# Kernel tuning notes

Hardware: AMD Instinct MI355X
Metric: run time of the kernel (lower is better)

The kernel has to match this reference:

```python
import jax, jax.numpy as jnp
import numpy as np

K, P, Q, D = 16, 1024, 1024, 64  # heads, value-in dim, out dim, head dim; P'=P, Q'=Q, D'=D
B, N = 2, 2048                   # batch, seq (self-attention: M=N)
TEMPERATURE = jnp.sqrt(jnp.float32(D))

def _xavier(key, shape):
    fan_in, fan_out = shape[-2], shape[-1]
    lim = jnp.sqrt(6.0 / (fan_in + fan_out))
    return jax.random.uniform(key, shape, jnp.float32, -lim, lim)

def setup_inputs() -> dict:
    key = jax.random.key(0)
    k0, k1, k2, k3, k4 = jax.random.split(key, 5)
    return {
        'y_prime': jax.random.normal(k0, (B, N, Q), jnp.float32),
        'mask': jnp.zeros((N, N), jnp.float32),  # log-domain additive mask [M,N]
        'Lam_x': _xavier(k1, (K, P, D)),  # Lambda^(x): [K,P',D']
        'Lam_y': _xavier(k2, (K, Q, D)),  # Lambda^(y): [K,Q',D']
        'Th_x': _xavier(k3, (K, P, D)),   # Theta^(x):  [K,P,D]
        'Th_y': _xavier(k4, (K, Q, D)),   # Theta^(y):  [K,Q,D]
    }

def reference(y_prime, mask, Lam_x, Lam_y, Th_x, Th_y):
    # self-attention: x' = x = y'
    x_p = y_prime
    x = x_p
    # key projection: [B,M,K,D']
    r = jnp.einsum('bmp,kpd->bmkd', x_p, Lam_x)
    # bilinear scores: [K,B,M,N]
    r = jnp.einsum('bmkd,kqd,bnq->kbmn', r, Lam_y, y_prime)
    r = r + mask[None, None, :, :]
    # softmax over M (axis=-2), scaled by sqrt(D')
    A = jax.nn.softmax(r / TEMPERATURE, axis=-2)
    # value aggregation: [B,N,K,D]
    r = jnp.einsum('kbmn,bmp,kpd->bnkd', A, x, Th_x)
    # output projection: [B,N,Q]
    return jnp.einsum('bnkd,kqd->bnq', r, Th_y)
```

## Files before the change

kernel.cpp:

```cpp
#include <hip/hip_runtime.h>
#include <hip/hip_bf16.h>

#define KH 16
#define PD 1024
#define QD 1024
#define DD 64
#define BB 2
#define NN 2048
#define BN 4096
#define ST 72
#define SOFT_C 12.0f
#define LOG2E 1.4426950408889634f
#define SOFT_C2 17.312340490667560f

typedef unsigned short u16;
typedef __attribute__((ext_vector_type(8))) short bf16x8;
typedef __attribute__((ext_vector_type(4))) short bf16x4;
typedef __attribute__((ext_vector_type(4))) float f32x4;

__device__ __forceinline__ float bf2f(u16 u) {
    return __uint_as_float(((unsigned)u) << 16);
}
__device__ __forceinline__ u16 f2bf(float f) {
    unsigned x = __float_as_uint(f);
    x += 0x7FFFu + ((x >> 16) & 1u);
    return (u16)(x >> 16);
}
__device__ __forceinline__ f32x4 mfma_k32(bf16x8 a, bf16x8 b, f32x4 c) {
    return __builtin_amdgcn_mfma_f32_16x16x32_bf16(a, b, c, 0, 0, 0);
}
__device__ __forceinline__ bf16x8 ldfrag(const u16* base, int r0, int kc, int lane) {
    return *reinterpret_cast<const bf16x8*>(base + (r0 + (lane & 15)) * ST + kc +
                                            ((lane >> 4) << 3));
}
__device__ __forceinline__ bf16x8 ldfragL(const u16* base, int r0, int kc, int lane) {
    return *reinterpret_cast<const bf16x8*>(base + ((r0 + (lane & 15)) << 6) + kc +
                                            ((lane >> 4) << 3));
}
__device__ __forceinline__ bf16x4 pack4(float a, float b, float c, float d) {
    union { bf16x4 v; __hip_bfloat162 h[2]; } u;
    u.h[0] = __float22bfloat162_rn(make_float2(a, b));
    u.h[1] = __float22bfloat162_rn(make_float2(c, d));
    return u.v;
}
__device__ __forceinline__ void gl_lds16(const u16* g, u16* l) {
    __builtin_amdgcn_global_load_lds(
        (const __attribute__((address_space(1))) void*)g,
        (__attribute__((address_space(3))) void*)l, 16, 0, 0);
}
template <int ROWS>
__device__ __forceinline__ void stage_dma(const u16* __restrict__ src, int ld,
                                          u16* dst, int lane, int w) {
#pragma unroll
    for (int c = 0; c < ROWS / 32; ++c) {
        int rbase = (w * (ROWS / 32) + c) * 8;
        const u16* g = src + (size_t)(rbase + (lane >> 3)) * ld + ((lane & 7) << 3);
        gl_lds16(g, dst + (rbase << 6));
    }
}

__global__ void detect_kernel(const u16* __restrict__ y, int* flag, int* mnz) {
    __shared__ int cnt;
    if (threadIdx.x == 0) cnt = 0;
    __syncthreads();
    int local = 0;
    for (int i = threadIdx.x; i < 8192; i += 256) {
        u16 u = y[i];
        int e = (u >> 7) & 0xFF;
        if (u == 0 || (e >= 96 && e < 160)) local++;
    }
    atomicAdd(&cnt, local);
    __syncthreads();
    if (threadIdx.x == 0) {
        *flag = (cnt > 7372) ? 1 : 0;
        *mnz = 0;
    }
}

__global__ __launch_bounds__(256) void prep_kernel(
    const void* __restrict__ ysrc, const void* __restrict__ msrc,
    const void* __restrict__ s0, const void* __restrict__ s1,
    const void* __restrict__ s2, const void* __restrict__ s3,
    u16* __restrict__ ycan, u16* __restrict__ LamXt, u16* __restrict__ LamYt,
    u16* __restrict__ ThXt, u16* __restrict__ ThYr, u16* __restrict__ maskc,
    const int* __restrict__ flag, int* __restrict__ mnz) {
    int z = blockIdx.z, bx = blockIdx.x, tid = threadIdx.x;
    int isbf = *flag;
    if (z == 0) {
        size_t n4 = (size_t)NN * NN / 8;
        if (!isbf) n4 *= 2;
        const uint4* p = (const uint4*)msrc;
        unsigned acc = 0;
        for (size_t i = (size_t)bx * 256 + tid; i < n4; i += 256 * 256) {
            uint4 v = p[i];
            acc |= v.x | v.y | v.z | v.w;
        }
        if (acc) atomicOr(mnz, 1);
    } else if (z == 1) {
        int n = BN * PD;
        for (int i = (bx * 256 + tid) * 4; i < n; i += 256 * 256 * 4) {
            if (isbf) {
                *reinterpret_cast<uint2*>(ycan + i) =
                    *reinterpret_cast<const uint2*>((const u16*)ysrc + i);
            } else {
                float4 f = *reinterpret_cast<const float4*>((const float*)ysrc + i);
                u16 t[4] = {f2bf(f.x), f2bf(f.y), f2bf(f.z), f2bf(f.w)};
                *reinterpret_cast<uint2*>(ycan + i) = *reinterpret_cast<uint2*>(t);
            }
        }
    } else if (z <= 4) {
        const void* src = (z == 2) ? s0 : (z == 3) ? s1 : s2;
        u16* dst = (z == 2) ? LamXt : (z == 3) ? LamYt : ThXt;
        float scale = (z == 3) ? 0.125f : 1.0f;
        int k = bx >> 4, p0 = (bx & 15) * 64;
        __shared__ float T[64][65];
        const u16* s16 = (const u16*)src + ((size_t)k * PD + p0) * DD;
        const float* s32 = (const float*)src + ((size_t)k * PD + p0) * DD;
#pragma unroll
        for (int it = 0; it < 2; ++it) {
            int chunk = it * 256 + tid;
            int row = chunk >> 3, c8 = (chunk & 7) << 3;
            float f[8];
            if (isbf) {
                uint4 v = *reinterpret_cast<const uint4*>(s16 + row * DD + c8);
                u16 t[8];
                *reinterpret_cast<uint4*>(t) = v;
#pragma unroll
                for (int e = 0; e < 8; ++e) f[e] = bf2f(t[e]);
            } else {
                float4 a = *reinterpret_cast<const float4*>(s32 + row * DD + c8);
                float4 b = *reinterpret_cast<const float4*>(s32 + row * DD + c8 + 4);
                f[0] = a.x; f[1] = a.y; f[2] = a.z; f[3] = a.w;
                f[4] = b.x; f[5] = b.y; f[6] = b.z; f[7] = b.w;
            }
#pragma unroll
            for (int e = 0; e < 8; ++e) T[row][c8 + e] = f[e] * scale;
        }
        __syncthreads();
        u16* drow = dst + (size_t)k * DD * PD + p0;
#pragma unroll
        for (int it = 0; it < 2; ++it) {
            int chunk = it * 256 + tid;
            int d = chunk >> 3, c8 = (chunk & 7) << 3;
            u16 t[8];
#pragma unroll
            for (int e = 0; e < 8; ++e) t[e] = f2bf(T[c8 + e][d]);
            *reinterpret_cast<uint4*>(drow + (size_t)d * PD + c8) =
                *reinterpret_cast<uint4*>(t);
        }
    } else if (z == 5) {
        int k = bx >> 4, q0 = (bx & 15) * 64;
#pragma unroll
        for (int it = 0; it < 2; ++it) {
            int chunk = it * 256 + tid;
            int row = chunk >> 3, c8 = (chunk & 7) << 3;
            size_t si = ((size_t)k * QD + q0 + row) * DD + c8;
            u16 t[8];
            if (isbf) {
                *reinterpret_cast<uint4*>(t) =
                    *reinterpret_cast<const uint4*>((const u16*)s3 + si);
            } else {
                float4 a = *reinterpret_cast<const float4*>((const float*)s3 + si);
                float4 b = *reinterpret_cast<const float4*>((const float*)s3 + si + 4);
                t[0] = f2bf(a.x); t[1] = f2bf(a.y); t[2] = f2bf(a.z); t[3] = f2bf(a.w);
                t[4] = f2bf(b.x); t[5] = f2bf(b.y); t[6] = f2bf(b.z); t[7] = f2bf(b.w);
            }
            *reinterpret_cast<uint4*>(ThYr + (size_t)(q0 + row) * (KH * DD) +
                                      k * DD + c8) = *reinterpret_cast<uint4*>(t);
        }
    } else {
        size_t n8 = (size_t)NN * NN / 8;
        for (size_t c = (size_t)bx * 256 + tid; c < n8; c += 256 * 256) {
            size_t i = c * 8;
            float f[8];
            if (isbf) {
                uint4 v = *reinterpret_cast<const uint4*>((const u16*)msrc + i);
                u16 t[8];
                *reinterpret_cast<uint4*>(t) = v;
#pragma unroll
                for (int e = 0; e < 8; ++e) f[e] = bf2f(t[e]);
            } else {
                float4 a = *reinterpret_cast<const float4*>((const float*)msrc + i);
                float4 b = *reinterpret_cast<const float4*>((const float*)msrc + i + 4);
                f[0] = a.x; f[1] = a.y; f[2] = a.z; f[3] = a.w;
                f[4] = b.x; f[5] = b.y; f[6] = b.z; f[7] = b.w;
            }
            u16 t[8];
#pragma unroll
            for (int e = 0; e < 8; ++e) t[e] = f2bf(f[e] * 0.125f);
            *reinterpret_cast<uint4*>(maskc + i) = *reinterpret_cast<uint4*>(t);
        }
    }
}

__global__ __launch_bounds__(256, 3) void proj_gemm(
    const u16* __restrict__ A,
    const u16* __restrict__ Bm,
    u16* __restrict__ Xk, u16* __restrict__ Yk, u16* __restrict__ Vtg) {
    int tid = threadIdx.x, lane = tid & 63, w = tid >> 6;
    int mhalf = w & 1, nhalf = w >> 1;
    int m0 = blockIdx.x * 128, n0 = blockIdx.y * 128;
    __shared__ u16 As[128 * 64];
    __shared__ u16 Bs[128 * 64];
    f32x4 acc[4][4] = {};

    for (int kk = 0; kk < PD; kk += 64) {
        __syncthreads();
        stage_dma<128>(A + (size_t)m0 * PD + kk, PD, As, lane, w);
        stage_dma<128>(Bm + (size_t)n0 * PD + kk, PD, Bs, lane, w);
        __syncthreads();
#pragma unroll
        for (int kc = 0; kc < 64; kc += 32) {
            bf16x8 af[4], bf[4];
#pragma unroll
            for (int i = 0; i < 4; ++i) af[i] = ldfragL(As, mhalf * 64 + i * 16, kc, lane);
#pragma unroll
            for (int j = 0; j < 4; ++j) bf[j] = ldfragL(Bs, nhalf * 64 + j * 16, kc, lane);
#pragma unroll
            for (int i = 0; i < 4; ++i)
#pragma unroll
                for (int j = 0; j < 4; ++j) acc[i][j] = mfma_k32(af[i], bf[j], acc[i][j]);
        }
    }
    int s = n0 >> 10;
    int quad = lane >> 4, col = lane & 15;
    u16* stg = nhalf ? Bs : As;
    __syncthreads();
    if (s == 2) {
#pragma unroll
        for (int i = 0; i < 4; ++i)
#pragma unroll
            for (int j = 0; j < 4; ++j)
                *reinterpret_cast<bf16x4*>(stg + ((mhalf * 2 + (i >> 1)) * 4 + j) * 512 +
                                           quad * 128 + col * 8 + (i & 1) * 4) =
                    pack4(acc[i][j][0], acc[i][j][1], acc[i][j][2], acc[i][j][3]);
    } else {
#pragma unroll
        for (int i = 0; i < 4; ++i)
#pragma unroll
            for (int j = 0; j < 4; ++j)
#pragma unroll
                for (int reg = 0; reg < 4; ++reg)
                    stg[(mhalf * 64 + i * 16 + quad * 4 + reg) * 64 + j * 16 + col] =
                        f2bf(acc[i][j][reg]);
    }
    __syncthreads();
#pragma unroll
    for (int h = 0; h < 2; ++h) {
        int kh = ((n0 + h * 64) >> 6) & 15;
        const u16* src = h ? Bs : As;
        if (s == 2) {
            u16* vb = Vtg + (size_t)kh * DD * BN + (size_t)m0 * 64;
#pragma unroll
            for (int it = 0; it < 4; ++it) {
                int chunk = it * 256 + tid;
                *reinterpret_cast<uint4*>(vb + chunk * 8) =
                    *reinterpret_cast<const uint4*>(src + chunk * 8);
            }
        } else {
            u16* ob = (s == 0 ? Xk : Yk) + (size_t)kh * BN * DD + (size_t)m0 * DD;
#pragma unroll
            for (int it = 0; it < 4; ++it) {
                int chunk = it * 256 + tid;
                *reinterpret_cast<uint4*>(ob + chunk * 8) =
                    *reinterpret_cast<const uint4*>(src + chunk * 8);
            }
        }
    }
}

__global__ __launch_bounds__(512, 4) void attn_kernel(
    const u16* __restrict__ Xk,
    const u16* __restrict__ Yk,
    const u16* __restrict__ Vtg,
    const u16* __restrict__ maskc,
    const int* __restrict__ mnz,
    u16* __restrict__ O) {
    int tid = threadIdx.x, lane = tid & 63, w = tid >> 6;
    int quad = lane >> 4, col = lane & 15;
    int H = blockIdx.x;
    int L = (H & 7) * 64 + (H >> 3);
    int q0 = (L & 15) * 128, k = (L >> 4) & 15, b = L >> 8;
    const u16* Qp = Yk + ((size_t)k * BN + b * NN + q0) * DD;
    const u16* Kp = Xk + ((size_t)k * BN + b * NN) * DD;
    const u16* Vh = Vtg + (size_t)k * DD * BN + (size_t)b * NN * 64;
    __shared__ u16 Kb[3][64 * ST];
    __shared__ u16 Ost[128 * ST];
    int mz = *mnz;

    const u16* qrow = Qp + (size_t)(w * 16 + col) * DD + (quad << 3);
    bf16x8 qf0 = *reinterpret_cast<const bf16x8*>(qrow);
    bf16x8 qf1 = *reinterpret_cast<const bf16x8*>(qrow + 32);

    int srow = tid >> 3, scol = (tid & 7) << 3;
    const u16* kgp = Kp + (size_t)srow * DD + scol;
    int soff = srow * ST + scol;

    uint4 kr = *reinterpret_cast<const uint4*>(kgp);
    *reinterpret_cast<uint4*>(Kb[0] + soff) = kr;
    kr = *reinterpret_cast<const uint4*>(kgp + (size_t)64 * DD);
    __syncthreads();

    float lp = 0.0f;
    f32x4 oacc[4] = {};

    for (int t = 0; t < 32; ++t) {
        int cur = t % 3;
        if (t < 31) {
            int nxt = (t + 1) % 3;
            *reinterpret_cast<uint4*>(Kb[nxt] + soff) = kr;
            __syncthreads();
        }
        const u16* Ks = Kb[cur];
        const u16* vt = Vh + t * 4096;
        bf16x8 av[2][4];
#pragma unroll
        for (int half = 0; half < 2; ++half)
#pragma unroll
            for (int dg = 0; dg < 4; ++dg)
                av[half][dg] = *reinterpret_cast<const bf16x8*>(
                    vt + half * 2048 + dg * 512 + lane * 8);
        if (t < 30) kr = *reinterpret_cast<const uint4*>(kgp + (size_t)(t + 2) * 64 * DD);
        int m0 = t * 64;

        bf16x4 pb4[4];
#pragma unroll
        for (int kg = 0; kg < 4; ++kg) {
            bf16x8 a0 = ldfrag(Ks, kg * 16, 0, lane);
            bf16x8 a1 = ldfrag(Ks, kg * 16, 32, lane);
            f32x4 s = {};
            s = mfma_k32(a0, qf0, s);
            s = mfma_k32(a1, qf1, s);
            if (mz) {
#pragma unroll
                for (int reg = 0; reg < 4; ++reg)
                    s[reg] += bf2f(
                        maskc[(size_t)(m0 + kg * 16 + quad * 4 + reg) * NN + q0 +
                              w * 16 + col]);
            }
            float p0 = exp2f(fmaf(s[0], LOG2E, -SOFT_C2));
            float p1 = exp2f(fmaf(s[1], LOG2E, -SOFT_C2));
            float p2 = exp2f(fmaf(s[2], LOG2E, -SOFT_C2));
            float p3 = exp2f(fmaf(s[3], LOG2E, -SOFT_C2));
            lp += (p0 + p1) + (p2 + p3);
            pb4[kg] = pack4(p0, p1, p2, p3);
        }
#pragma unroll
        for (int half = 0; half < 2; ++half) {
            bf16x8 pb8 = __builtin_shufflevector(pb4[half * 2], pb4[half * 2 + 1],
                                                 0, 1, 2, 3, 4, 5, 6, 7);
#pragma unroll
            for (int dg = 0; dg < 4; ++dg)
                oacc[dg] = mfma_k32(av[half][dg], pb8, oacc[dg]);
        }
    }

    float l = lp;
    l += __shfl_xor(l, 16);
    l += __shfl_xor(l, 32);
    float inv = 1.0f / l;
    int q = w * 16 + col;
#pragma unroll
    for (int dg = 0; dg < 4; ++dg)
        *reinterpret_cast<bf16x4*>(Ost + q * ST + dg * 16 + quad * 4) =
            pack4(oacc[dg][0] * inv, oacc[dg][1] * inv, oacc[dg][2] * inv,
                  oacc[dg][3] * inv);
    __syncthreads();
#pragma unroll
    for (int it = 0; it < 2; ++it) {
        int chunk = it * 512 + tid;
        int row = chunk >> 3, c8 = (chunk & 7) << 3;
        *reinterpret_cast<uint4*>(O + (size_t)(b * NN + q0 + row) * (KH * DD) +
                                  k * DD + c8) =
            *reinterpret_cast<const uint4*>(Ost + row * ST + c8);
    }
}

__global__ __launch_bounds__(256, 3) void out_gemm(
    const u16* __restrict__ A,
    const u16* __restrict__ Bm,
    const int* __restrict__ flag,
    void* __restrict__ outv) {
    int tid = threadIdx.x, lane = tid & 63, w = tid >> 6;
    int mhalf = w & 1, nhalf = w >> 1;
    int m0 = blockIdx.x * 128, n0 = blockIdx.y * 128;
    __shared__ u16 S[2][128 * 64];
    u16* As = S[0];
    u16* Bs = S[1];
    f32x4 acc[4][4] = {};

    for (int kk = 0; kk < KH * DD; kk += 64) {
        __syncthreads();
        stage_dma<128>(A + (size_t)m0 * (KH * DD) + kk, KH * DD, As, lane, w);
        stage_dma<128>(Bm + (size_t)n0 * (KH * DD) + kk, KH * DD, Bs, lane, w);
        __syncthreads();
#pragma unroll
        for (int kc = 0; kc < 64; kc += 32) {
            bf16x8 af[4], bf[4];
#pragma unroll
            for (int i = 0; i < 4; ++i) af[i] = ldfragL(As, mhalf * 64 + i * 16, kc, lane);
#pragma unroll
            for (int j = 0; j < 4; ++j) bf[j] = ldfragL(Bs, nhalf * 64 + j * 16, kc, lane);
#pragma unroll
            for (int i = 0; i < 4; ++i)
#pragma unroll
                for (int j = 0; j < 4; ++j) acc[i][j] = mfma_k32(af[i], bf[j], acc[i][j]);
        }
    }
    int isbf = *flag;
    int quad = lane >> 4, col = lane & 15;
    if (isbf) {
#pragma unroll
        for (int i = 0; i < 4; ++i)
#pragma unroll
            for (int j = 0; j < 4; ++j)
#pragma unroll
                for (int reg = 0; reg < 4; ++reg) {
                    size_t row = m0 + mhalf * 64 + i * 16 + quad * 4 + reg;
                    int c = n0 + nhalf * 64 + j * 16 + col;
                    ((u16*)outv)[row * QD + c] = f2bf(acc[i][j][reg]);
                }
    } else {
        float* Sf = (float*)&S[0][0];
#pragma unroll
        for (int h = 0; h < 2; ++h) {
            __syncthreads();
            if (mhalf == h) {
#pragma unroll
                for (int i = 0; i < 4; ++i)
#pragma unroll
                    for (int j = 0; j < 4; ++j)
#pragma unroll
                        for (int reg = 0; reg < 4; ++reg)
                            Sf[(i * 16 + quad * 4 + reg) * 128 + nhalf * 64 +
                               j * 16 + col] = acc[i][j][reg];
            }
            __syncthreads();
            float* orow = (float*)outv + (size_t)(m0 + h * 64) * QD + n0;
#pragma unroll
            for (int it = 0; it < 8; ++it) {
                int chunk = it * 256 + tid;
                int row = chunk >> 5, c4 = (chunk & 31) * 4;
                *reinterpret_cast<float4*>(orow + (size_t)row * QD + c4) =
                    *reinterpret_cast<const float4*>(Sf + row * 128 + c4);
            }
        }
    }
}

extern "C" void kernel_launch(void* const* d_in, const int* in_sizes, int n_in,
                              void* d_out, int out_size, void* d_ws, size_t ws_size,
                              hipStream_t stream) {
    char* wsb = (char*)d_ws;
    int* flag = (int*)wsb;
    int* mnz = (int*)(wsb + 16);
    u16* ycan = (u16*)(wsb + 64);
    const size_t NYP = (size_t)BN * PD;
    const size_t NW = (size_t)KH * PD * DD;
    const size_t OSZ = (size_t)BN * KH * DD;
    u16* Wcat = ycan + NYP;
    u16* ThYr = Wcat + 3 * NW;
    u16* Xk = ThYr + NW;
    u16* Yk = Xk + OSZ;
    u16* Vtg = Yk + OSZ;
    u16* maskc = Vtg + OSZ;
    u16* Ob = ycan;

    detect_kernel<<<1, 256, 0, stream>>>((const u16*)d_in[0], flag, mnz);
    prep_kernel<<<dim3(256, 1, 7), 256, 0, stream>>>(
        d_in[0], d_in[1], d_in[2], d_in[3], d_in[4], d_in[5], ycan, Wcat,
        Wcat + NW, Wcat + 2 * NW, ThYr, maskc, flag, mnz);
    proj_gemm<<<dim3(BN / 128, 3072 / 128), 256, 0, stream>>>(ycan, Wcat, Xk, Yk, Vtg);
    attn_kernel<<<512, 512, 0, stream>>>(Xk, Yk, Vtg, maskc, mnz, Ob);
    out_gemm<<<dim3(BN / 128, QD / 128), 256, 0, stream>>>(Ob, ThYr, flag, d_out);
}
```

Before: 234.2 us.

## Split mask scan, skip zero-mask conversion, shrink attention blocks, raise MFMA priority

Mask-nonzero detection moves into its own kernel that runs before prep, so prep can skip converting the mask when it is all zero. When the input is already bf16, prep skips copying y and proj_gemm reads the source directly. The attention kernel goes from 512-thread blocks covering 128 queries to 256-thread blocks covering 64 queries, with twice as many blocks. Each thread now stages two K rows per tile, and setprio is raised around the PV MFMAs. This trades an extra launch and more K re-reads for less conversion traffic and finer-grained attention scheduling.

Result: no change. 230.9 us (-1.4%).

```diff
diff --git a/kernel.cpp b/kernel.cpp
--- a/kernel.cpp
+++ b/kernel.cpp
@@ -77,41 +77,41 @@
     }
 }
 
+__global__ __launch_bounds__(256) void scan_kernel(const void* __restrict__ msrc,
+                                                   const int* __restrict__ flag,
+                                                   int* __restrict__ mnz) {
+    size_t n4 = (size_t)NN * NN / 8;
+    if (!*flag) n4 *= 2;
+    const uint4* p = (const uint4*)msrc;
+    unsigned acc = 0;
+    for (size_t i = (size_t)blockIdx.x * 256 + threadIdx.x; i < n4; i += 256 * 256) {
+        uint4 v = p[i];
+        acc |= v.x | v.y | v.z | v.w;
+    }
+    if (acc) atomicOr(mnz, 1);
+}
+
 __global__ __launch_bounds__(256) void prep_kernel(
     const void* __restrict__ ysrc, const void* __restrict__ msrc,
     const void* __restrict__ s0, const void* __restrict__ s1,
     const void* __restrict__ s2, const void* __restrict__ s3,
     u16* __restrict__ ycan, u16* __restrict__ LamXt, u16* __restrict__ LamYt,
     u16* __restrict__ ThXt, u16* __restrict__ ThYr, u16* __restrict__ maskc,
-    const int* __restrict__ flag, int* __restrict__ mnz) {
+    const int* __restrict__ flag, const int* __restrict__ mnz) {
     int z = blockIdx.z, bx = blockIdx.x, tid = threadIdx.x;
     int isbf = *flag;
     if (z == 0) {
-        size_t n4 = (size_t)NN * NN / 8;
-        if (!isbf) n4 *= 2;
-        const uint4* p = (const uint4*)msrc;
-        unsigned acc = 0;
-        for (size_t i = (size_t)bx * 256 + tid; i < n4; i += 256 * 256) {
-            uint4 v = p[i];
-            acc |= v.x | v.y | v.z | v.w;
-        }
-        if (acc) atomicOr(mnz, 1);
-    } else if (z == 1) {
+        if (isbf) return;
         int n = BN * PD;
         for (int i = (bx * 256 + tid) * 4; i < n; i += 256 * 256 * 4) {
-            if (isbf) {
-                *reinterpret_cast<uint2*>(ycan + i) =
-                    *reinterpret_cast<const uint2*>((const u16*)ysrc + i);
-            } else {
-                float4 f = *reinterpret_cast<const float4*>((const float*)ysrc + i);
-                u16 t[4] = {f2bf(f.x), f2bf(f.y), f2bf(f.z), f2bf(f.w)};
-                *reinterpret_cast<uint2*>(ycan + i) = *reinterpret_cast<uint2*>(t);
-            }
-        }
-    } else if (z <= 4) {
-        const void* src = (z == 2) ? s0 : (z == 3) ? s1 : s2;
-        u16* dst = (z == 2) ? LamXt : (z == 3) ? LamYt : ThXt;
-        float scale = (z == 3) ? 0.125f : 1.0f;
+            float4 f = *reinterpret_cast<const float4*>((const float*)ysrc + i);
+            u16 t[4] = {f2bf(f.x), f2bf(f.y), f2bf(f.z), f2bf(f.w)};
+            *reinterpret_cast<uint2*>(ycan + i) = *reinterpret_cast<uint2*>(t);
+        }
+    } else if (z <= 3) {
+        const void* src = (z == 1) ? s0 : (z == 2) ? s1 : s2;
+        u16* dst = (z == 1) ? LamXt : (z == 2) ? LamYt : ThXt;
+        float scale = (z == 2) ? 0.125f : 1.0f;
         int k = bx >> 4, p0 = (bx & 15) * 64;
         __shared__ float T[64][65];
         const u16* s16 = (const u16*)src + ((size_t)k * PD + p0) * DD;
@@ -148,7 +148,7 @@
             *reinterpret_cast<uint4*>(drow + (size_t)d * PD + c8) =
                 *reinterpret_cast<uint4*>(t);
         }
-    } else if (z == 5) {
+    } else if (z == 4) {
         int k = bx >> 4, q0 = (bx & 15) * 64;
 #pragma unroll
         for (int it = 0; it < 2; ++it) {
@@ -169,6 +169,7 @@
                                       k * DD + c8) = *reinterpret_cast<uint4*>(t);
         }
     } else {
+        if (*mnz == 0) return;
         size_t n8 = (size_t)NN * NN / 8;
         for (size_t c = (size_t)bx * 256 + tid; c < n8; c += 256 * 256) {
             size_t i = c * 8;
@@ -194,12 +195,15 @@
 }
 
 __global__ __launch_bounds__(256, 3) void proj_gemm(
-    const u16* __restrict__ A,
+    const u16* __restrict__ Acan,
+    const void* __restrict__ ysrc,
+    const int* __restrict__ flag,
     const u16* __restrict__ Bm,
     u16* __restrict__ Xk, u16* __restrict__ Yk, u16* __restrict__ Vtg) {
     int tid = threadIdx.x, lane = tid & 63, w = tid >> 6;
     int mhalf = w & 1, nhalf = w >> 1;
     int m0 = blockIdx.x * 128, n0 = blockIdx.y * 128;
+    const u16* A = (*flag) ? (const u16*)ysrc : Acan;
     __shared__ u16 As[128 * 64];
     __shared__ u16 Bs[128 * 64];
     f32x4 acc[4][4] = {};
@@ -269,7 +273,7 @@
     }
 }
 
-__global__ __launch_bounds__(512, 4) void attn_kernel(
+__global__ __launch_bounds__(256, 4) void attn_kernel(
     const u16* __restrict__ Xk,
     const u16* __restrict__ Yk,
     const u16* __restrict__ Vtg,
@@ -279,13 +283,13 @@
     int tid = threadIdx.x, lane = tid & 63, w = tid >> 6;
     int quad = lane >> 4, col = lane & 15;
     int H = blockIdx.x;
-    int L = (H & 7) * 64 + (H >> 3);
-    int q0 = (L & 15) * 128, k = (L >> 4) & 15, b = L >> 8;
+    int L = (H & 7) * 128 + (H >> 3);
+    int q0 = (L & 31) * 64, k = (L >> 5) & 15, b = L >> 9;
     const u16* Qp = Yk + ((size_t)k * BN + b * NN + q0) * DD;
     const u16* Kp = Xk + ((size_t)k * BN + b * NN) * DD;
     const u16* Vh = Vtg + (size_t)k * DD * BN + (size_t)b * NN * 64;
     __shared__ u16 Kb[3][64 * ST];
-    __shared__ u16 Ost[128 * ST];
+    __shared__ u16 Ost[64 * ST];
     int mz = *mnz;
 
     const u16* qrow = Qp + (size_t)(w * 16 + col) * DD + (quad << 3);
@@ -296,9 +300,12 @@
     const u16* kgp = Kp + (size_t)srow * DD + scol;
     int soff = srow * ST + scol;
 
-    uint4 kr = *reinterpret_cast<const uint4*>(kgp);
-    *reinterpret_cast<uint4*>(Kb[0] + soff) = kr;
-    kr = *reinterpret_cast<const uint4*>(kgp + (size_t)64 * DD);
+    uint4 kr0 = *reinterpret_cast<const uint4*>(kgp);
+    uint4 kr1 = *reinterpret_cast<const uint4*>(kgp + (size_t)32 * DD);
+    *reinterpret_cast<uint4*>(Kb[0] + soff) = kr0;
+    *reinterpret_cast<uint4*>(Kb[0] + soff + 32 * ST) = kr1;
+    kr0 = *reinterpret_cast<const uint4*>(kgp + (size_t)64 * DD);
+    kr1 = *reinterpret_cast<const uint4*>(kgp + (size_t)96 * DD);
     __syncthreads();
 
     float lp = 0.0f;
@@ -308,19 +315,24 @@
         int cur = t % 3;
         if (t < 31) {
             int nxt = (t + 1) % 3;
-            *reinterpret_cast<uint4*>(Kb[nxt] + soff) = kr;
+            *reinterpret_cast<uint4*>(Kb[nxt] + soff) = kr0;
+            *reinterpret_cast<uint4*>(Kb[nxt] + soff + 32 * ST) = kr1;
             __syncthreads();
         }
         const u16* Ks = Kb[cur];
         const u16* vt = Vh + t * 4096;
         bf16x8 av[2][4];
 #pragma unroll
-        for (int half = 0; half < 2; ++half)
+        for (int hlf = 0; hlf < 2; ++hlf)
 #pragma unroll
             for (int dg = 0; dg < 4; ++dg)
-                av[half][dg] = *reinterpret_cast<const bf16x8*>(
-                    vt + half * 2048 + dg * 512 + lane * 8);
-        if (t < 30) kr = *reinterpret_cast<const uint4*>(kgp + (size_t)(t + 2) * 64 * DD);
+                av[hlf][dg] = *reinterpret_cast<const bf16x8*>(
+                    vt + hlf * 2048 + dg * 512 + lane * 8);
+        if (t < 30) {
+            const u16* knb = kgp + (size_t)(t + 2) * 64 * DD;
+            kr0 = *reinterpret_cast<const uint4*>(knb);
+            kr1 = *reinterpret_cast<const uint4*>(knb + (size_t)32 * DD);
+        }
         int m0 = t * 64;
 
         bf16x4 pb4[4];
@@ -345,14 +357,16 @@
             lp += (p0 + p1) + (p2 + p3);
             pb4[kg] = pack4(p0, p1, p2, p3);
         }
-#pragma unroll
-        for (int half = 0; half < 2; ++half) {
-            bf16x8 pb8 = __builtin_shufflevector(pb4[half * 2], pb4[half * 2 + 1],
+        __builtin_amdgcn_s_setprio(1);
+#pragma unroll
+        for (int hlf = 0; hlf < 2; ++hlf) {
+            bf16x8 pb8 = __builtin_shufflevector(pb4[hlf * 2], pb4[hlf * 2 + 1],
                                                  0, 1, 2, 3, 4, 5, 6, 7);
 #pragma unroll
             for (int dg = 0; dg < 4; ++dg)
-                oacc[dg] = mfma_k32(av[half][dg], pb8, oacc[dg]);
-        }
+                oacc[dg] = mfma_k32(av[hlf][dg], pb8, oacc[dg]);
+        }
+        __builtin_amdgcn_s_setprio(0);
     }
 
     float l = lp;
@@ -368,7 +382,7 @@
     __syncthreads();
 #pragma unroll
     for (int it = 0; it < 2; ++it) {
-        int chunk = it * 512 + tid;
+        int chunk = it * 256 + tid;
         int row = chunk >> 3, c8 = (chunk & 7) << 3;
         *reinterpret_cast<uint4*>(O + (size_t)(b * NN + q0 + row) * (KH * DD) +
                                   k * DD + c8) =
@@ -467,10 +481,12 @@
     u16* Ob = ycan;
 
     detect_kernel<<<1, 256, 0, stream>>>((const u16*)d_in[0], flag, mnz);
-    prep_kernel<<<dim3(256, 1, 7), 256, 0, stream>>>(
+    scan_kernel<<<256, 256, 0, stream>>>(d_in[1], flag, mnz);
+    prep_kernel<<<dim3(256, 1, 6), 256, 0, stream>>>(
         d_in[0], d_in[1], d_in[2], d_in[3], d_in[4], d_in[5], ycan, Wcat,
         Wcat + NW, Wcat + 2 * NW, ThYr, maskc, flag, mnz);
-    proj_gemm<<<dim3(BN / 128, 3072 / 128), 256, 0, stream>>>(ycan, Wcat, Xk, Yk, Vtg);
-    attn_kernel<<<512, 512, 0, stream>>>(Xk, Yk, Vtg, maskc, mnz, Ob);
+    proj_gemm<<<dim3(BN / 128, 3072 / 128), 256, 0, stream>>>(
+        ycan, d_in[0], flag, Wcat, Xk, Yk, Vtg);
+    attn_kernel<<<1024, 256, 0, stream>>>(Xk, Yk, Vtg, maskc, mnz, Ob);
     out_gemm<<<dim3(BN / 128, QD / 128), 256, 0, stream>>>(Ob, ThYr, flag, d_out);
 }
```
